# Performance work log

Measured on AMD Instinct MI355X. Metric: run time of the kernel, lower is better.

## Reference

```python
import jax, jax.numpy as jnp
import numpy as np

B, N, D = 8, 2048, 64          # batch, n_pts, latent_ndim
K, S = 8, 256                   # n_clusters, book_size
TEMP = 0.5
EPS = 1e-10


def _gumbel(key, shape):
    U = jax.random.uniform(key, shape, dtype=jnp.float32)
    return -jnp.log(-jnp.log(U + EPS) + EPS)


def setup_inputs() -> dict:
    key = jax.random.key(0)
    k1, k2, k3 = jax.random.split(key, 3)
    return {
        "ze": jax.random.normal(k1, (B, N, D), jnp.float32),
        "c_logits": jax.random.normal(k2, (B, K), jnp.float32),
        "books": jax.random.normal(k3, (K, S, D), jnp.float32),
        "log_param_q": jnp.float32(0.0),       # log(param_q_init=1.0)
        "log_param_q_cls": jnp.float32(0.0),
        "is_train": 1,
    }


def reference(ze, c_logits, books, log_param_q, log_param_q_cls, is_train):
    b, n_pts, d = ze.shape
    k, s, _ = books.shape
    precision_q = 0.5 / jnp.clip(1.0 + jnp.exp(log_param_q), 1e-10)

    # pairwise squared distances: (b, k, n_pts, book_size)
    dist = ((ze ** 2).sum(-1)[:, None, :, None]
            + (books ** 2).sum(-1)[None, :, None, :]
            - 2.0 * jnp.einsum("bnd,ksd->bkns", ze, books))
    logit_k = -dist * precision_q  # (b, k, n, s)

    if is_train:
        precision_q_cls = 0.5 / jnp.clip(1.0 + jnp.exp(log_param_q_cls), 1e-10)
        nkey = jax.random.key(42)
        g_cls = _gumbel(jax.random.fold_in(nkey, 0), (b, k))
        g_enc = _gumbel(jax.random.fold_in(nkey, 1), (b, k, n_pts, s))
        # gumbel-softmax over clusters
        c_prob = jax.nn.softmax((c_logits * precision_q_cls + g_cls) / TEMP, axis=-1)  # (b,k)
        # mixture of per-cluster logits
        logits = jnp.einsum("bkns,bk->bns", logit_k, c_prob)
        # gumbel-softmax relaxed codebook assignment per cluster
        enc = jax.nn.softmax((logit_k + g_enc) / TEMP, axis=-1)  # (b,k,n,s)
        zq = jnp.einsum("bkns,ksd,bk->bnd", enc, books, c_prob)
    else:
        idx = jnp.argmax(c_logits, axis=-1)                 # (b,)
        sel_books = books[idx]                              # (b,s,d)
        logits = jnp.take_along_axis(logit_k, idx[:, None, None, None], axis=1)[:, 0]  # (b,n,s)
        code = jnp.argmax(logits, axis=-1)                  # (b,n)
        zq = jnp.take_along_axis(sel_books, code[..., None], axis=1)  # hard lookup (b,n,d)

    prob = jax.nn.softmax(logits, axis=-1)
    log_prob = jax.nn.log_softmax(logits, axis=-1)
    return zq, precision_q, prob, log_prob
```

## Files before the change

### kernel.cpp

```cpp
#include <hip/hip_runtime.h>
#include <cstdint>
#include <cstddef>


#define B_ 8
#define N_ 2048
#define D_ 64
#define K_ 8
#define S_ 256
#define ROWS 32

#define ZQ_ELEMS   (B_ * N_ * D_)
#define PROB_ELEMS (B_ * N_ * S_)

typedef __attribute__((ext_vector_type(8))) short short8;
typedef __attribute__((ext_vector_type(4))) float f32x4;

struct U2 { unsigned a, b; };

__host__ __device__ constexpr U2 tf2x32(unsigned k0, unsigned k1, unsigned x0, unsigned x1) {
  unsigned ks2 = k0 ^ k1 ^ 0x1BD11BDAu;
#define TFR(r) x0 += x1; x1 = (x1 << (r)) | (x1 >> (32 - (r))); x1 ^= x0;
  x0 += k0; x1 += k1;
  TFR(13) TFR(15) TFR(26) TFR(6)
  x0 += k1;  x1 += ks2 + 1u;
  TFR(17) TFR(29) TFR(16) TFR(24)
  x0 += ks2; x1 += k0 + 2u;
  TFR(13) TFR(15) TFR(26) TFR(6)
  x0 += k0;  x1 += k1 + 3u;
  TFR(17) TFR(29) TFR(16) TFR(24)
  x0 += k1;  x1 += ks2 + 4u;
  TFR(13) TFR(15) TFR(26) TFR(6)
  x0 += ks2; x1 += k0 + 5u;
#undef TFR
  return U2{x0, x1};
}

constexpr U2 KCLS = tf2x32(0u, 42u, 0u, 0u);
constexpr U2 KENC = tf2x32(0u, 42u, 0u, 1u);

__device__ __forceinline__ unsigned tf_bits(unsigned k0, unsigned k1, unsigned i) {
  U2 r = tf2x32(k0, k1, 0u, i);
  return r.a ^ r.b;
}

__device__ __forceinline__ float bits_to_u01(unsigned bits) {
  return __uint_as_float((bits >> 9) | 0x3f800000u) - 1.0f;
}

__device__ __forceinline__ unsigned short f2bf(float f) {
  unsigned u = __float_as_uint(f);
  unsigned r = (u + 0x7FFFu + ((u >> 16) & 1u)) >> 16;
  return (unsigned short)r;
}
__device__ __forceinline__ float bf2f(unsigned short h) {
  return __uint_as_float(((unsigned)h) << 16);
}

__global__ void k_cvt(const float* __restrict__ books,
                      ushort* __restrict__ bkhi, ushort* __restrict__ bklo,
                      ushort* __restrict__ bkT) {
  const int t4 = blockIdx.x * 256 + threadIdx.x;
  float4 v = ((const float4*)books)[t4];
  const int flat = t4 * 4;
  const int k = flat >> 14, s = (flat >> 6) & 255, d = flat & 63;
  float f[4] = {v.x, v.y, v.z, v.w};
  ushort4 hh, ll;
  ushort* hp = (ushort*)&hh; ushort* lp = (ushort*)&ll;
  #pragma unroll
  for (int i = 0; i < 4; ++i) {
    unsigned short hb = f2bf(f[i]);
    hp[i] = hb;
    lp[i] = f2bf(f[i] - bf2f(hb));
  }
  *(ushort4*)(bkhi + flat) = hh;
  *(ushort4*)(bklo + flat) = ll;
  #pragma unroll
  for (int i = 0; i < 4; ++i)
    bkT[(((k * 64) + d + i) << 8) + s] = f2bf(f[i]);
}

__global__ void k_misc(const float* __restrict__ books,
                       const float* __restrict__ c_logits,
                       const float* __restrict__ lpq,
                       const float* __restrict__ lpq_cls,
                       float* __restrict__ pq_out,
                       float* __restrict__ cprob_ws,
                       float* __restrict__ b2_ws) {
  if (blockIdx.x < 8) {
    const int t = blockIdx.x * 256 + threadIdx.x;
    const float4* p = (const float4*)(books + (size_t)t * D_);
    float s = 0.0f;
    #pragma unroll
    for (int i = 0; i < 16; ++i) {
      float4 v = p[i];
      s += v.x * v.x + v.y * v.y + v.z * v.z + v.w * v.w;
    }
    b2_ws[t] = s;
  } else {
    const int t = threadIdx.x;
    __shared__ float g[64];
    if (t == 0) pq_out[0] = 0.5f / fmaxf(1.0f + expf(lpq[0]), 1e-10f);
    const float pq_cls = 0.5f / fmaxf(1.0f + expf(lpq_cls[0]), 1e-10f);
    if (t < 64) {
      unsigned bits = tf_bits(KCLS.a, KCLS.b, (unsigned)t);
      float u = bits_to_u01(bits);
      g[t] = -logf(-logf(u + 1e-10f) + 1e-10f);
    }
    __syncthreads();
    if (t < 64) {
      float v = (c_logits[t] * pq_cls + g[t]) * 2.0f;
      float M = v;
      #pragma unroll
      for (int m = 1; m < 8; m <<= 1) M = fmaxf(M, __shfl_xor(M, m, 8));
      float e = expf(v - M);
      float Z = e;
      #pragma unroll
      for (int m = 1; m < 8; m <<= 1) Z += __shfl_xor(Z, m, 8);
      cprob_ws[t] = e / Z;
    }
  }
}

__global__ __launch_bounds__(512, 4) void k_main(
    const float* __restrict__ ze,
    const ushort* __restrict__ bkhi, const ushort* __restrict__ bklo,
    const ushort* __restrict__ bkT,
    const float* __restrict__ lpq, const float* __restrict__ cprob_ws,
    const float* __restrict__ b2_ws,
    float* __restrict__ zq_out, float* __restrict__ prob_out,
    float* __restrict__ logp_out) {

  __shared__ __align__(16) ushort zeh_s[ROWS][72];
  __shared__ __align__(16) ushort zel_s[ROWS][72];
  __shared__ __align__(16) ushort enc_s[ROWS][264];
  __shared__ __align__(16) float b2_s[K_ * S_];
  __shared__ float red_s[ROWS][4];
  __shared__ float m_s[ROWS][4];
  __shared__ float z_s[ROWS][4];
  __shared__ float q2_s[ROWS];
  __shared__ float cp_s[8];

  const int tid = threadIdx.x;
  const int b   = blockIdx.y;
  const int n0  = blockIdx.x * ROWS;
  const int w   = tid >> 6;
  const int l   = tid & 63;
  const int llo = l & 15;
  const int lhi = l >> 4;
  const int h   = w & 1;
  const int sq  = w >> 1;
  const int s0  = sq * 64;
  const int d0  = sq * 16;

  const float pq = 0.5f / fmaxf(1.0f + expf(lpq[0]), 1e-10f);

  {
    const int row = tid >> 4, d4 = (tid & 15) * 4;
    float4 v = *(const float4*)(ze + ((size_t)(b * N_ + n0 + row)) * D_ + d4);
    float q = v.x * v.x + v.y * v.y + v.z * v.z + v.w * v.w;
    q += __shfl_xor(q, 1); q += __shfl_xor(q, 2);
    q += __shfl_xor(q, 4); q += __shfl_xor(q, 8);
    if ((tid & 15) == 0) q2_s[row] = q;
    float f[4] = {v.x, v.y, v.z, v.w};
    ushort4 hh, ll4;
    ushort* hp = (ushort*)&hh; ushort* lp = (ushort*)&ll4;
    #pragma unroll
    for (int i = 0; i < 4; ++i) {
      unsigned short hb = f2bf(f[i]);
      hp[i] = hb;
      lp[i] = f2bf(f[i] - bf2f(hb));
    }
    *(ushort4*)&zeh_s[row][d4] = hh;
    *(ushort4*)&zel_s[row][d4] = ll4;
  }
  #pragma unroll
  for (int i = 0; i < 4; ++i) b2_s[tid + i * 512] = b2_ws[tid + i * 512];
  if (tid < 8) cp_s[tid] = cprob_ws[b * 8 + tid];
  __syncthreads();

  const short8 ah0 = *(const short8*)&zeh_s[h * 16 + llo][lhi * 8];
  const short8 ah1 = *(const short8*)&zeh_s[h * 16 + llo][32 + lhi * 8];
  const short8 al0 = *(const short8*)&zel_s[h * 16 + llo][lhi * 8];
  const short8 al1 = *(const short8*)&zel_s[h * 16 + llo][32 + lhi * 8];

  float lacc[4][4];
  #pragma unroll
  for (int nt = 0; nt < 4; ++nt)
    #pragma unroll
    for (int r = 0; r < 4; ++r) lacc[nt][r] = 0.0f;
  f32x4 zqacc = {0.f, 0.f, 0.f, 0.f};

  for (int cb = 0; cb < K_; ++cb) {
    const ushort* bh = bkhi + cb * (S_ * D_);
    const ushort* bl = bklo + cb * (S_ * D_);

    f32x4 acc[4];
    #pragma unroll
    for (int nt = 0; nt < 4; ++nt) acc[nt] = (f32x4){0.f, 0.f, 0.f, 0.f};
    #pragma unroll
    for (int nt = 0; nt < 4; ++nt) {
      const ushort* bp = bh + (size_t)(s0 + nt * 16 + llo) * D_ + lhi * 8;
      const ushort* bq = bl + (size_t)(s0 + nt * 16 + llo) * D_ + lhi * 8;
      short8 b0 = *(const short8*)bp;
      short8 b1 = *(const short8*)(bp + 32);
      short8 c0 = *(const short8*)bq;
      short8 c1 = *(const short8*)(bq + 32);
      acc[nt] = __builtin_amdgcn_mfma_f32_16x16x32_bf16(ah0, b0, acc[nt], 0, 0, 0);
      acc[nt] = __builtin_amdgcn_mfma_f32_16x16x32_bf16(ah1, b1, acc[nt], 0, 0, 0);
      acc[nt] = __builtin_amdgcn_mfma_f32_16x16x32_bf16(al0, b0, acc[nt], 0, 0, 0);
      acc[nt] = __builtin_amdgcn_mfma_f32_16x16x32_bf16(al1, b1, acc[nt], 0, 0, 0);
      acc[nt] = __builtin_amdgcn_mfma_f32_16x16x32_bf16(ah0, c0, acc[nt], 0, 0, 0);
      acc[nt] = __builtin_amdgcn_mfma_f32_16x16x32_bf16(ah1, c1, acc[nt], 0, 0, 0);
    }

    const float cpk = cp_s[cb];
    float b2v[4];
    #pragma unroll
    for (int nt = 0; nt < 4; ++nt)
      b2v[nt] = b2_s[cb * 256 + s0 + nt * 16 + llo];
    float ev[4][4];
    #pragma unroll
    for (int r = 0; r < 4; ++r) {
      const int rowg = h * 16 + lhi * 4 + r;
      const float q2 = q2_s[rowg];
      const unsigned ib =
          (((unsigned)(b * 8 + cb)) << 19) | (((unsigned)(n0 + rowg)) << 8);
      float Zp = 0.0f;
      #pragma unroll
      for (int nt = 0; nt < 4; ++nt) {
        float dist = q2 + b2v[nt] - 2.0f * acc[nt][r];
        float lk = -pq * dist;
        lacc[nt][r] = fmaf(cpk, lk, lacc[nt][r]);
        unsigned bits = tf_bits(KENC.a, KENC.b, ib | (unsigned)(s0 + nt * 16 + llo));
        float u = bits_to_u01(bits);
        float wv = 0.0f - __logf(u + 1e-10f);
        float t = wv + 1e-10f;
        float ex = __expf(fmaf(2.0f, lk, 40.0f));
        float e = __fdividef(ex, t * t);
        ev[r][nt] = e;
        Zp += e;
      }
      Zp += __shfl_xor(Zp, 1); Zp += __shfl_xor(Zp, 2);
      Zp += __shfl_xor(Zp, 4); Zp += __shfl_xor(Zp, 8);
      if (llo == 0) red_s[rowg][sq] = Zp;
    }
    __syncthreads();

    #pragma unroll
    for (int r = 0; r < 4; ++r) {
      const int rowg = h * 16 + lhi * 4 + r;
      float Z = (red_s[rowg][0] + red_s[rowg][1]) +
                (red_s[rowg][2] + red_s[rowg][3]);
      const float sc = __fdividef(cpk, Z);
      #pragma unroll
      for (int nt = 0; nt < 4; ++nt)
        enc_s[rowg][s0 + nt * 16 + llo] = f2bf(ev[r][nt] * sc);
    }
    __syncthreads();

    {
      const ushort* bt = bkT + (size_t)cb * (D_ * S_) + (size_t)(d0 + llo) * S_ + lhi * 8;
      #pragma unroll
      for (int sc = 0; sc < 8; ++sc) {
        short8 af = *(const short8*)&enc_s[h * 16 + llo][sc * 32 + lhi * 8];
        short8 bf = *(const short8*)(bt + sc * 32);
        zqacc = __builtin_amdgcn_mfma_f32_16x16x32_bf16(af, bf, zqacc, 0, 0, 0);
      }
    }
    __syncthreads();
  }

  #pragma unroll
  for (int r = 0; r < 4; ++r)
    zq_out[((size_t)(b * N_ + n0 + h * 16 + lhi * 4 + r)) * D_ + d0 + llo] = zqacc[r];

  #pragma unroll
  for (int r = 0; r < 4; ++r) {
    const int rowg = h * 16 + lhi * 4 + r;
    float Mp = fmaxf(fmaxf(lacc[0][r], lacc[1][r]), fmaxf(lacc[2][r], lacc[3][r]));
    Mp = fmaxf(Mp, __shfl_xor(Mp, 1)); Mp = fmaxf(Mp, __shfl_xor(Mp, 2));
    Mp = fmaxf(Mp, __shfl_xor(Mp, 4)); Mp = fmaxf(Mp, __shfl_xor(Mp, 8));
    if (llo == 0) m_s[rowg][sq] = Mp;
  }
  __syncthreads();
  float Mfull[4];
  #pragma unroll
  for (int r = 0; r < 4; ++r) {
    const int rowg = h * 16 + lhi * 4 + r;
    const float M = fmaxf(fmaxf(m_s[rowg][0], m_s[rowg][1]),
                          fmaxf(m_s[rowg][2], m_s[rowg][3]));
    Mfull[r] = M;
    float Zp = 0.0f;
    #pragma unroll
    for (int nt = 0; nt < 4; ++nt) Zp += __expf(lacc[nt][r] - M);
    Zp += __shfl_xor(Zp, 1); Zp += __shfl_xor(Zp, 2);
    Zp += __shfl_xor(Zp, 4); Zp += __shfl_xor(Zp, 8);
    if (llo == 0) z_s[rowg][sq] = Zp;
  }
  __syncthreads();
  #pragma unroll
  for (int r = 0; r < 4; ++r) {
    const int rowg = h * 16 + lhi * 4 + r;
    const float M = Mfull[r];
    float Z = (z_s[rowg][0] + z_s[rowg][1]) + (z_s[rowg][2] + z_s[rowg][3]);
    const float inv = __fdividef(1.0f, Z);
    const float lZ = __logf(Z);
    const size_t base = ((size_t)(b * N_ + n0 + rowg)) * S_ + s0 + llo;
    #pragma unroll
    for (int nt = 0; nt < 4; ++nt) {
      const float lmm = lacc[nt][r] - M;
      prob_out[base + nt * 16] = __expf(lmm) * inv;
      logp_out[base + nt * 16] = lmm - lZ;
    }
  }
}

extern "C" void kernel_launch(void* const* d_in, const int* in_sizes, int n_in,
                              void* d_out, int out_size, void* d_ws, size_t ws_size,
                              hipStream_t stream) {
  const float* ze    = (const float*)d_in[0];
  const float* clog  = (const float*)d_in[1];
  const float* books = (const float*)d_in[2];
  const float* lpq   = (const float*)d_in[3];
  const float* lpqc  = (const float*)d_in[4];

  float* out      = (float*)d_out;
  float* zq_out   = out;
  float* pq_out   = out + ZQ_ELEMS;
  float* prob_out = out + ZQ_ELEMS + 1;
  float* logp_out = out + ZQ_ELEMS + 1 + PROB_ELEMS;

  float* wsf    = (float*)d_ws;
  float* cprob  = wsf;
  float* b2     = wsf + 64;
  ushort* bkhi  = (ushort*)(wsf + 2112);
  ushort* bklo  = bkhi + (K_ * S_ * D_);
  ushort* bkT   = bklo + (K_ * S_ * D_);

  hipLaunchKernelGGL(k_cvt, dim3(128), dim3(256), 0, stream, books, bkhi, bklo, bkT);
  hipLaunchKernelGGL(k_misc, dim3(9), dim3(256), 0, stream,
                     books, clog, lpq, lpqc, pq_out, cprob, b2);
  hipLaunchKernelGGL(k_main, dim3(64, 8), dim3(512), 0, stream,
                     ze, bkhi, bklo, bkT, lpq, cprob, b2, zq_out, prob_out, logp_out);
}
```

Measured before the change: 221.5 us.

## Halve row tile, split codebook work across eight waves, and merge prep kernels

The main kernel now processes 16 rows per block instead of 32, with each of the eight waves owning 32 codebook columns. Each zq tile is split across two waves along the codebook axis and summed through shared memory, and the launch grid doubles with a higher occupancy hint. The two preprocessing kernels are merged into one that computes book norms, bf16 hi/lo splits, and a transpose staged through LDS with coalesced stores, saving a launch and the strided scatter writes. The Threefry rotate now uses a builtin. The trade-off is more blocks, each reloading codebook data from L2, plus an extra LDS reduction for zq.

```diff
diff --git a/kernel.cpp b/kernel.cpp
--- a/kernel.cpp
+++ b/kernel.cpp
@@ -8,7 +8,7 @@
 #define D_ 64
 #define K_ 8
 #define S_ 256
-#define ROWS 32
+#define ROWS 16
 
 #define ZQ_ELEMS   (B_ * N_ * D_)
 #define PROB_ELEMS (B_ * N_ * S_)
@@ -40,8 +40,22 @@
 constexpr U2 KENC = tf2x32(0u, 42u, 0u, 1u);
 
 __device__ __forceinline__ unsigned tf_bits(unsigned k0, unsigned k1, unsigned i) {
-  U2 r = tf2x32(k0, k1, 0u, i);
-  return r.a ^ r.b;
+  unsigned ks2 = k0 ^ k1 ^ 0x1BD11BDAu;
+  unsigned x0 = 0u, x1 = i;
+#define TFRD(r) x0 += x1; x1 = __builtin_rotateleft32(x1, r); x1 ^= x0;
+  x0 += k0; x1 += k1;
+  TFRD(13) TFRD(15) TFRD(26) TFRD(6)
+  x0 += k1;  x1 += ks2 + 1u;
+  TFRD(17) TFRD(29) TFRD(16) TFRD(24)
+  x0 += ks2; x1 += k0 + 2u;
+  TFRD(13) TFRD(15) TFRD(26) TFRD(6)
+  x0 += k0;  x1 += k1 + 3u;
+  TFRD(17) TFRD(29) TFRD(16) TFRD(24)
+  x0 += k1;  x1 += ks2 + 4u;
+  TFRD(13) TFRD(15) TFRD(26) TFRD(6)
+  x0 += ks2; x1 += k0 + 5u;
+#undef TFRD
+  return x0 ^ x1;
 }
 
 __device__ __forceinline__ float bits_to_u01(unsigned bits) {
@@ -57,59 +71,75 @@
   return __uint_as_float(((unsigned)h) << 16);
 }
 
-__global__ void k_cvt(const float* __restrict__ books,
-                      ushort* __restrict__ bkhi, ushort* __restrict__ bklo,
-                      ushort* __restrict__ bkT) {
-  const int t4 = blockIdx.x * 256 + threadIdx.x;
-  float4 v = ((const float4*)books)[t4];
-  const int flat = t4 * 4;
-  const int k = flat >> 14, s = (flat >> 6) & 255, d = flat & 63;
-  float f[4] = {v.x, v.y, v.z, v.w};
-  ushort4 hh, ll;
-  ushort* hp = (ushort*)&hh; ushort* lp = (ushort*)&ll;
-  #pragma unroll
-  for (int i = 0; i < 4; ++i) {
-    unsigned short hb = f2bf(f[i]);
-    hp[i] = hb;
-    lp[i] = f2bf(f[i] - bf2f(hb));
-  }
-  *(ushort4*)(bkhi + flat) = hh;
-  *(ushort4*)(bklo + flat) = ll;
-  #pragma unroll
-  for (int i = 0; i < 4; ++i)
-    bkT[(((k * 64) + d + i) << 8) + s] = f2bf(f[i]);
-}
-
-__global__ void k_misc(const float* __restrict__ books,
+__global__ void k_prep(const float* __restrict__ books,
                        const float* __restrict__ c_logits,
                        const float* __restrict__ lpq,
                        const float* __restrict__ lpq_cls,
                        float* __restrict__ pq_out,
                        float* __restrict__ cprob_ws,
-                       float* __restrict__ b2_ws) {
-  if (blockIdx.x < 8) {
-    const int t = blockIdx.x * 256 + threadIdx.x;
-    const float4* p = (const float4*)(books + (size_t)t * D_);
-    float s = 0.0f;
+                       float* __restrict__ b2_ws,
+                       ushort* __restrict__ bkhi, ushort* __restrict__ bklo,
+                       ushort* __restrict__ bkT) {
+  __shared__ ushort lds_t[64][68];
+  __shared__ float g[64];
+  const int tid = threadIdx.x;
+
+  if (blockIdx.x < 32) {
+    const int kk = blockIdx.x >> 2;
+    const int st0 = (blockIdx.x & 3) * 64;
+    const int sl = tid >> 2, dq = tid & 3;
+    const float* src = books + ((size_t)(kk * 256 + st0 + sl)) * D_ + dq * 16;
+    float f[16];
+    #pragma unroll
+    for (int j = 0; j < 4; ++j) {
+      float4 v = *(const float4*)(src + j * 4);
+      f[j*4+0] = v.x; f[j*4+1] = v.y; f[j*4+2] = v.z; f[j*4+3] = v.w;
+    }
+    float q = 0.0f;
+    #pragma unroll
+    for (int i = 0; i < 16; ++i) q = fmaf(f[i], f[i], q);
+    q += __shfl_xor(q, 1); q += __shfl_xor(q, 2);
+    if (dq == 0) b2_ws[kk * 256 + st0 + sl] = q;
+
+    ushort hi[16], lo[16];
     #pragma unroll
     for (int i = 0; i < 16; ++i) {
-      float4 v = p[i];
-      s += v.x * v.x + v.y * v.y + v.z * v.z + v.w * v.w;
-    }
-    b2_ws[t] = s;
+      hi[i] = f2bf(f[i]);
+      lo[i] = f2bf(f[i] - bf2f(hi[i]));
+    }
+    const size_t obase = ((size_t)(kk * 256 + st0 + sl)) * D_ + dq * 16;
+    #pragma unroll
+    for (int j = 0; j < 4; ++j) {
+      ushort4 h4, l4;
+      h4.x = hi[j*4+0]; h4.y = hi[j*4+1]; h4.z = hi[j*4+2]; h4.w = hi[j*4+3];
+      l4.x = lo[j*4+0]; l4.y = lo[j*4+1]; l4.z = lo[j*4+2]; l4.w = lo[j*4+3];
+      *(ushort4*)(bkhi + obase + j * 4) = h4;
+      *(ushort4*)(bklo + obase + j * 4) = l4;
+      *(ushort4*)&lds_t[sl][dq * 16 + j * 4] = h4;
+    }
+    __syncthreads();
+    const int dl = tid >> 2, s4 = tid & 3;
+    ushort* dst = bkT + ((size_t)(kk * 64 + dl)) * S_ + st0 + s4 * 16;
+    #pragma unroll
+    for (int j = 0; j < 4; ++j) {
+      ushort4 o;
+      o.x = lds_t[s4*16 + j*4 + 0][dl];
+      o.y = lds_t[s4*16 + j*4 + 1][dl];
+      o.z = lds_t[s4*16 + j*4 + 2][dl];
+      o.w = lds_t[s4*16 + j*4 + 3][dl];
+      *(ushort4*)(dst + j * 4) = o;
+    }
   } else {
-    const int t = threadIdx.x;
-    __shared__ float g[64];
-    if (t == 0) pq_out[0] = 0.5f / fmaxf(1.0f + expf(lpq[0]), 1e-10f);
+    if (tid == 0) pq_out[0] = 0.5f / fmaxf(1.0f + expf(lpq[0]), 1e-10f);
     const float pq_cls = 0.5f / fmaxf(1.0f + expf(lpq_cls[0]), 1e-10f);
-    if (t < 64) {
-      unsigned bits = tf_bits(KCLS.a, KCLS.b, (unsigned)t);
+    if (tid < 64) {
+      unsigned bits = tf_bits(KCLS.a, KCLS.b, (unsigned)tid);
       float u = bits_to_u01(bits);
-      g[t] = -logf(-logf(u + 1e-10f) + 1e-10f);
-    }
-    __syncthreads();
-    if (t < 64) {
-      float v = (c_logits[t] * pq_cls + g[t]) * 2.0f;
+      g[tid] = -logf(-logf(u + 1e-10f) + 1e-10f);
+    }
+    __syncthreads();
+    if (tid < 64) {
+      float v = (c_logits[tid] * pq_cls + g[tid]) * 2.0f;
       float M = v;
       #pragma unroll
       for (int m = 1; m < 8; m <<= 1) M = fmaxf(M, __shfl_xor(M, m, 8));
@@ -117,12 +147,12 @@
       float Z = e;
       #pragma unroll
       for (int m = 1; m < 8; m <<= 1) Z += __shfl_xor(Z, m, 8);
-      cprob_ws[t] = e / Z;
-    }
-  }
-}
-
-__global__ __launch_bounds__(512, 4) void k_main(
+      cprob_ws[tid] = e / Z;
+    }
+  }
+}
+
+__global__ __launch_bounds__(512, 8) void k_main(
     const float* __restrict__ ze,
     const ushort* __restrict__ bkhi, const ushort* __restrict__ bklo,
     const ushort* __restrict__ bkT,
@@ -135,9 +165,10 @@
   __shared__ __align__(16) ushort zel_s[ROWS][72];
   __shared__ __align__(16) ushort enc_s[ROWS][264];
   __shared__ __align__(16) float b2_s[K_ * S_];
-  __shared__ float red_s[ROWS][4];
-  __shared__ float m_s[ROWS][4];
-  __shared__ float z_s[ROWS][4];
+  __shared__ __align__(16) float red_s[ROWS][8];
+  __shared__ __align__(16) float m_s[ROWS][8];
+  __shared__ __align__(16) float z_s[ROWS][8];
+  __shared__ __align__(16) float zq_red[ROWS][68];
   __shared__ float q2_s[ROWS];
   __shared__ float cp_s[8];
 
@@ -148,14 +179,13 @@
   const int l   = tid & 63;
   const int llo = l & 15;
   const int lhi = l >> 4;
-  const int h   = w & 1;
-  const int sq  = w >> 1;
-  const int s0  = sq * 64;
-  const int d0  = sq * 16;
+  const int s0  = w * 32;
+  const int d0  = (w >> 1) * 16;
+  const int sh  = w & 1;
 
   const float pq = 0.5f / fmaxf(1.0f + expf(lpq[0]), 1e-10f);
 
-  {
+  if (tid < 256) {
     const int row = tid >> 4, d4 = (tid & 15) * 4;
     float4 v = *(const float4*)(ze + ((size_t)(b * N_ + n0 + row)) * D_ + d4);
     float q = v.x * v.x + v.y * v.y + v.z * v.z + v.w * v.w;
@@ -174,38 +204,40 @@
     *(ushort4*)&zeh_s[row][d4] = hh;
     *(ushort4*)&zel_s[row][d4] = ll4;
   }
-  #pragma unroll
-  for (int i = 0; i < 4; ++i) b2_s[tid + i * 512] = b2_ws[tid + i * 512];
+  {
+    float4 bv = *(const float4*)(b2_ws + tid * 4);
+    *(float4*)&b2_s[tid * 4] = bv;
+  }
   if (tid < 8) cp_s[tid] = cprob_ws[b * 8 + tid];
   __syncthreads();
 
-  const short8 ah0 = *(const short8*)&zeh_s[h * 16 + llo][lhi * 8];
-  const short8 ah1 = *(const short8*)&zeh_s[h * 16 + llo][32 + lhi * 8];
-  const short8 al0 = *(const short8*)&zel_s[h * 16 + llo][lhi * 8];
-  const short8 al1 = *(const short8*)&zel_s[h * 16 + llo][32 + lhi * 8];
-
-  float lacc[4][4];
+  const short8 ah0 = *(const short8*)&zeh_s[llo][lhi * 8];
+  const short8 ah1 = *(const short8*)&zeh_s[llo][32 + lhi * 8];
+  const short8 al0 = *(const short8*)&zel_s[llo][lhi * 8];
+  const short8 al1 = *(const short8*)&zel_s[llo][32 + lhi * 8];
+
+  float lacc[2][4];
   #pragma unroll
-  for (int nt = 0; nt < 4; ++nt)
+  for (int nt = 0; nt < 2; ++nt)
     #pragma unroll
     for (int r = 0; r < 4; ++r) lacc[nt][r] = 0.0f;
   f32x4 zqacc = {0.f, 0.f, 0.f, 0.f};
 
   for (int cb = 0; cb < K_; ++cb) {
-    const ushort* bh = bkhi + cb * (S_ * D_);
-    const ushort* bl = bklo + cb * (S_ * D_);
-
-    f32x4 acc[4];
-    #pragma unroll
-    for (int nt = 0; nt < 4; ++nt) acc[nt] = (f32x4){0.f, 0.f, 0.f, 0.f};
-    #pragma unroll
-    for (int nt = 0; nt < 4; ++nt) {
-      const ushort* bp = bh + (size_t)(s0 + nt * 16 + llo) * D_ + lhi * 8;
-      const ushort* bq = bl + (size_t)(s0 + nt * 16 + llo) * D_ + lhi * 8;
-      short8 b0 = *(const short8*)bp;
-      short8 b1 = *(const short8*)(bp + 32);
-      short8 c0 = *(const short8*)bq;
-      short8 c1 = *(const short8*)(bq + 32);
+    const ushort* bp = bkhi + cb * (S_ * D_) + (size_t)(s0 + llo) * D_ + lhi * 8;
+    const ushort* bq = bklo + cb * (S_ * D_) + (size_t)(s0 + llo) * D_ + lhi * 8;
+
+    f32x4 acc[2];
+    acc[0] = (f32x4){0.f, 0.f, 0.f, 0.f};
+    acc[1] = (f32x4){0.f, 0.f, 0.f, 0.f};
+    #pragma unroll
+    for (int nt = 0; nt < 2; ++nt) {
+      const ushort* p = bp + nt * (16 * D_);
+      const ushort* q = bq + nt * (16 * D_);
+      short8 b0 = *(const short8*)p;
+      short8 b1 = *(const short8*)(p + 32);
+      short8 c0 = *(const short8*)q;
+      short8 c1 = *(const short8*)(q + 32);
       acc[nt] = __builtin_amdgcn_mfma_f32_16x16x32_bf16(ah0, b0, acc[nt], 0, 0, 0);
       acc[nt] = __builtin_amdgcn_mfma_f32_16x16x32_bf16(ah1, b1, acc[nt], 0, 0, 0);
       acc[nt] = __builtin_amdgcn_mfma_f32_16x16x32_bf16(al0, b0, acc[nt], 0, 0, 0);
@@ -215,20 +247,19 @@
     }
 
     const float cpk = cp_s[cb];
-    float b2v[4];
-    #pragma unroll
-    for (int nt = 0; nt < 4; ++nt)
-      b2v[nt] = b2_s[cb * 256 + s0 + nt * 16 + llo];
-    float ev[4][4];
+    float b2v[2];
+    b2v[0] = b2_s[cb * 256 + s0 + llo];
+    b2v[1] = b2_s[cb * 256 + s0 + 16 + llo];
+    float ev[4][2];
     #pragma unroll
     for (int r = 0; r < 4; ++r) {
-      const int rowg = h * 16 + lhi * 4 + r;
+      const int rowg = lhi * 4 + r;
       const float q2 = q2_s[rowg];
       const unsigned ib =
           (((unsigned)(b * 8 + cb)) << 19) | (((unsigned)(n0 + rowg)) << 8);
       float Zp = 0.0f;
       #pragma unroll
-      for (int nt = 0; nt < 4; ++nt) {
+      for (int nt = 0; nt < 2; ++nt) {
         float dist = q2 + b2v[nt] - 2.0f * acc[nt][r];
         float lk = -pq * dist;
         lacc[nt][r] = fmaf(cpk, lk, lacc[nt][r]);
@@ -243,28 +274,29 @@
       }
       Zp += __shfl_xor(Zp, 1); Zp += __shfl_xor(Zp, 2);
       Zp += __shfl_xor(Zp, 4); Zp += __shfl_xor(Zp, 8);
-      if (llo == 0) red_s[rowg][sq] = Zp;
+      if (llo == 0) red_s[rowg][w] = Zp;
     }
     __syncthreads();
 
     #pragma unroll
     for (int r = 0; r < 4; ++r) {
-      const int rowg = h * 16 + lhi * 4 + r;
-      float Z = (red_s[rowg][0] + red_s[rowg][1]) +
-                (red_s[rowg][2] + red_s[rowg][3]);
+      const int rowg = lhi * 4 + r;
+      const float4 z0 = *(const float4*)&red_s[rowg][0];
+      const float4 z1 = *(const float4*)&red_s[rowg][4];
+      float Z = ((z0.x + z0.y) + (z0.z + z0.w)) + ((z1.x + z1.y) + (z1.z + z1.w));
       const float sc = __fdividef(cpk, Z);
+      enc_s[rowg][s0 + llo]      = f2bf(ev[r][0] * sc);
+      enc_s[rowg][s0 + 16 + llo] = f2bf(ev[r][1] * sc);
+    }
+    __syncthreads();
+
+    {
+      const ushort* bt = bkT + (size_t)cb * (D_ * S_) +
+                         (size_t)(d0 + llo) * S_ + sh * 128 + lhi * 8;
       #pragma unroll
-      for (int nt = 0; nt < 4; ++nt)
-        enc_s[rowg][s0 + nt * 16 + llo] = f2bf(ev[r][nt] * sc);
-    }
-    __syncthreads();
-
-    {
-      const ushort* bt = bkT + (size_t)cb * (D_ * S_) + (size_t)(d0 + llo) * S_ + lhi * 8;
-      #pragma unroll
-      for (int sc = 0; sc < 8; ++sc) {
-        short8 af = *(const short8*)&enc_s[h * 16 + llo][sc * 32 + lhi * 8];
-        short8 bf = *(const short8*)(bt + sc * 32);
+      for (int sc4 = 0; sc4 < 4; ++sc4) {
+        short8 af = *(const short8*)&enc_s[llo][sh * 128 + sc4 * 32 + lhi * 8];
+        short8 bf = *(const short8*)(bt + sc4 * 32);
         zqacc = __builtin_amdgcn_mfma_f32_16x16x32_bf16(af, bf, zqacc, 0, 0, 0);
       }
     }
@@ -272,43 +304,46 @@
   }
 
   #pragma unroll
-  for (int r = 0; r < 4; ++r)
-    zq_out[((size_t)(b * N_ + n0 + h * 16 + lhi * 4 + r)) * D_ + d0 + llo] = zqacc[r];
-
-  #pragma unroll
   for (int r = 0; r < 4; ++r) {
-    const int rowg = h * 16 + lhi * 4 + r;
-    float Mp = fmaxf(fmaxf(lacc[0][r], lacc[1][r]), fmaxf(lacc[2][r], lacc[3][r]));
+    const int rowg = lhi * 4 + r;
+    if (sh == 0) zq_red[rowg][d0 + llo] = zqacc[r];
+    float Mp = fmaxf(lacc[0][r], lacc[1][r]);
     Mp = fmaxf(Mp, __shfl_xor(Mp, 1)); Mp = fmaxf(Mp, __shfl_xor(Mp, 2));
     Mp = fmaxf(Mp, __shfl_xor(Mp, 4)); Mp = fmaxf(Mp, __shfl_xor(Mp, 8));
-    if (llo == 0) m_s[rowg][sq] = Mp;
+    if (llo == 0) m_s[rowg][w] = Mp;
   }
   __syncthreads();
   float Mfull[4];
   #pragma unroll
   for (int r = 0; r < 4; ++r) {
-    const int rowg = h * 16 + lhi * 4 + r;
-    const float M = fmaxf(fmaxf(m_s[rowg][0], m_s[rowg][1]),
-                          fmaxf(m_s[rowg][2], m_s[rowg][3]));
+    const int rowg = lhi * 4 + r;
+    const float4 m0 = *(const float4*)&m_s[rowg][0];
+    const float4 m1 = *(const float4*)&m_s[rowg][4];
+    const float M = fmaxf(fmaxf(fmaxf(m0.x, m0.y), fmaxf(m0.z, m0.w)),
+                          fmaxf(fmaxf(m1.x, m1.y), fmaxf(m1.z, m1.w)));
     Mfull[r] = M;
-    float Zp = 0.0f;
-    #pragma unroll
-    for (int nt = 0; nt < 4; ++nt) Zp += __expf(lacc[nt][r] - M);
+    float Zp = __expf(lacc[0][r] - M) + __expf(lacc[1][r] - M);
     Zp += __shfl_xor(Zp, 1); Zp += __shfl_xor(Zp, 2);
     Zp += __shfl_xor(Zp, 4); Zp += __shfl_xor(Zp, 8);
-    if (llo == 0) z_s[rowg][sq] = Zp;
+    if (llo == 0) z_s[rowg][w] = Zp;
+    if (sh == 1) {
+      float vzq = zq_red[rowg][d0 + llo] + zqacc[r];
+      zq_out[((size_t)(b * N_ + n0 + rowg)) * D_ + d0 + llo] = vzq;
+    }
   }
   __syncthreads();
   #pragma unroll
   for (int r = 0; r < 4; ++r) {
-    const int rowg = h * 16 + lhi * 4 + r;
+    const int rowg = lhi * 4 + r;
     const float M = Mfull[r];
-    float Z = (z_s[rowg][0] + z_s[rowg][1]) + (z_s[rowg][2] + z_s[rowg][3]);
+    const float4 z0 = *(const float4*)&z_s[rowg][0];
+    const float4 z1 = *(const float4*)&z_s[rowg][4];
+    float Z = ((z0.x + z0.y) + (z0.z + z0.w)) + ((z1.x + z1.y) + (z1.z + z1.w));
     const float inv = __fdividef(1.0f, Z);
     const float lZ = __logf(Z);
     const size_t base = ((size_t)(b * N_ + n0 + rowg)) * S_ + s0 + llo;
     #pragma unroll
-    for (int nt = 0; nt < 4; ++nt) {
+    for (int nt = 0; nt < 2; ++nt) {
       const float lmm = lacc[nt][r] - M;
       prob_out[base + nt * 16] = __expf(lmm) * inv;
       logp_out[base + nt * 16] = lmm - lZ;
@@ -338,9 +373,8 @@
   ushort* bklo  = bkhi + (K_ * S_ * D_);
   ushort* bkT   = bklo + (K_ * S_ * D_);
 
-  hipLaunchKernelGGL(k_cvt, dim3(128), dim3(256), 0, stream, books, bkhi, bklo, bkT);
-  hipLaunchKernelGGL(k_misc, dim3(9), dim3(256), 0, stream,
-                     books, clog, lpq, lpqc, pq_out, cprob, b2);
-  hipLaunchKernelGGL(k_main, dim3(64, 8), dim3(512), 0, stream,
+  hipLaunchKernelGGL(k_prep, dim3(33), dim3(256), 0, stream,
+                     books, clog, lpq, lpqc, pq_out, cprob, b2, bkhi, bklo, bkT);
+  hipLaunchKernelGGL(k_main, dim3(128, 8), dim3(512), 0, stream,
                      ze, bkhi, bklo, bkT, lpq, cprob, b2, zq_out, prob_out, logp_out);
 }
```

New measurement: 240.2 us. 1.08x slower.
